# Optimization experiments

Measured on AMD Instinct MI355X. Metric: run time of the kernel, lower is better.

The kernel has to match this reference:

```python
import jax, jax.numpy as jnp
import numpy as np

N_ATOMS = 131072
N_ELEM = 4
D_IN = 128
D_HID = 256
D_OUT = 1


def setup_inputs() -> dict:
    key = jax.random.key(0)
    k1, k2, k3, k4, k5, k6 = jax.random.split(key, 6)
    descriptors = jax.random.normal(k1, (N_ATOMS, D_IN), dtype=jnp.float32)
    element_ids = jax.random.randint(k2, (N_ATOMS,), 0, N_ELEM, dtype=jnp.int32)
    # per-element 2-layer MLP params, stacked over the element (expert) axis
    s1 = 1.0 / np.sqrt(D_IN)
    s2 = 1.0 / np.sqrt(D_HID)
    W1 = jax.random.uniform(k3, (N_ELEM, D_IN, D_HID), minval=-s1, maxval=s1, dtype=jnp.float32)
    b1 = jax.random.uniform(k4, (N_ELEM, D_HID), minval=-s1, maxval=s1, dtype=jnp.float32)
    W2 = jax.random.uniform(k5, (N_ELEM, D_HID, D_OUT), minval=-s2, maxval=s2, dtype=jnp.float32)
    b2 = jax.random.uniform(k6, (N_ELEM, D_OUT), minval=-s2, maxval=s2, dtype=jnp.float32)
    return {"descriptors": descriptors, "element_ids": element_ids,
            "W1": W1, "b1": b1, "W2": W2, "b2": b2}


def reference(descriptors, element_ids, W1, b1, W2, b2):
    # Dense all-expert compute then per-atom select (E is tiny, avoids
    # materializing a per-atom gathered [N, D_IN, D_HID] weight tensor).
    h = jnp.tanh(jnp.einsum('ni,eih->neh', descriptors, W1) + b1[None])  # [N,E,H]
    y = jnp.einsum('neh,eho->neo', h, W2) + b2[None]                      # [N,E,O]
    idx = element_ids.astype(jnp.int32)[:, None, None]                    # [N,1,1]
    per_atom = jnp.take_along_axis(y, idx, axis=1)[:, 0, :]               # [N,O]
    total_energy = per_atom.sum(axis=0)                                   # [O]
    return total_energy
```

## Files before the change

### kernel.cpp

```cpp
#include <hip/hip_runtime.h>
#include <hip/hip_bf16.h>
#include <stdint.h>

#define N_ATOMS 131072
#define D_IN    128
#define D_HID   256
#define N_ELEM  4
#define NPAD    (N_ATOMS + N_ELEM * 64)
#define K4_BLOCKS 512
#define HIST_BLOCKS 128

typedef __attribute__((ext_vector_type(8))) short bf16x8;
typedef __attribute__((ext_vector_type(4))) float f32x4;
typedef unsigned long long ull;

#define WS_BPART  262272
#define WS_BCNT   278784
#define WS_SIDX   287232

__device__ __forceinline__ unsigned short f2bf_rne(float f) {
    union { float f; unsigned u; } v; v.f = f;
    unsigned r = v.u + 0x7FFFu + ((v.u >> 16) & 1u);
    return (unsigned short)(r >> 16);
}

__device__ __forceinline__ bf16x8 cvt8(f32x4 v0, f32x4 v1) {
    uint4 o;
    o.x = (__float_as_uint(v0[0]) >> 16) | (__float_as_uint(v0[1]) & 0xFFFF0000u);
    o.y = (__float_as_uint(v0[2]) >> 16) | (__float_as_uint(v0[3]) & 0xFFFF0000u);
    o.z = (__float_as_uint(v1[0]) >> 16) | (__float_as_uint(v1[1]) & 0xFFFF0000u);
    o.w = (__float_as_uint(v1[2]) >> 16) | (__float_as_uint(v1[3]) & 0xFFFF0000u);
    return __builtin_bit_cast(bf16x8, o);
}

__device__ __forceinline__ int4 wave_reduce4(int4 v) {
    #pragma unroll
    for (int off = 32; off; off >>= 1) {
        v.x += __shfl_xor(v.x, off);
        v.y += __shfl_xor(v.y, off);
        v.z += __shfl_xor(v.z, off);
        v.w += __shfl_xor(v.w, off);
    }
    return v;
}

__device__ __forceinline__ ull same_expert_mask(int e) {
    ull m0 = __ballot(e & 1);
    ull m1 = __ballot(e & 2);
    ull m = (e & 1) ? m0 : ~m0;
    return m & ((e & 2) ? m1 : ~m1);
}

__global__ void tnn_k1_fused(const int* __restrict__ eid, int* __restrict__ bcnt,
                             const float* __restrict__ W1, unsigned short* __restrict__ W1t) {
    __shared__ float tile[64][65];
    __shared__ int lc[N_ELEM];
    int t = threadIdx.x;
    if (blockIdx.x < 32) {
        int b  = blockIdx.x;
        int e  = b >> 3;
        int k0 = ((b >> 2) & 1) * 64;
        int h0 = (b & 3) * 64;
        int cg = t & 15;
        int rr = t >> 4;
        const float* src = W1 + ((size_t)e * D_IN + k0) * D_HID + h0;
        #pragma unroll
        for (int j = 0; j < 4; ++j) {
            int row = rr + j * 16;
            f32x4 v = *(const f32x4*)(src + (size_t)row * D_HID + cg * 4);
            tile[row][cg * 4 + 0] = v[0];
            tile[row][cg * 4 + 1] = v[1];
            tile[row][cg * 4 + 2] = v[2];
            tile[row][cg * 4 + 3] = v[3];
        }
        __syncthreads();
        unsigned short* dst = W1t + ((size_t)e * D_HID + h0) * D_IN + k0;
        #pragma unroll
        for (int j = 0; j < 4; ++j) {
            int hrow = rr + j * 16;
            ushort4 o;
            o.x = f2bf_rne(tile[cg * 4 + 0][hrow]);
            o.y = f2bf_rne(tile[cg * 4 + 1][hrow]);
            o.z = f2bf_rne(tile[cg * 4 + 2][hrow]);
            o.w = f2bf_rne(tile[cg * 4 + 3][hrow]);
            *(ushort4*)(dst + (size_t)hrow * D_IN + cg * 4) = o;
        }
    } else {
        int hb = blockIdx.x - 32;
        int lane = t & 63;
        if (t < N_ELEM) lc[t] = 0;
        __syncthreads();
        int base = hb * 1024;
        #pragma unroll
        for (int r = 0; r < 4; ++r) {
            int e = eid[base + r * 256 + t];
            ull m = same_expert_mask(e);
            if (lane == __builtin_ctzll(m))
                atomicAdd(&lc[e], __popcll(m));
        }
        __syncthreads();
        if (t < N_ELEM) bcnt[hb * 4 + t] = lc[t];
    }
}

__global__ void tnn_k3_scatter(const int* __restrict__ eid, const int* __restrict__ bcnt,
                               int* __restrict__ sortedIdx) {
    __shared__ int lc[N_ELEM];
    __shared__ int base4[N_ELEM];
    int t = threadIdx.x;
    int b = blockIdx.x;
    int lane = t & 63;
    if (t < N_ELEM) lc[t] = 0;
    if (t < 64) {
        int4 cl = ((const int4*)bcnt)[t];
        int4 ch = ((const int4*)bcnt)[t + 64];
        int4 tot = {cl.x + ch.x, cl.y + ch.y, cl.z + ch.z, cl.w + ch.w};
        tot = wave_reduce4(tot);
        int4 pre = {(t < b) ? cl.x : 0, (t < b) ? cl.y : 0,
                    (t < b) ? cl.z : 0, (t < b) ? cl.w : 0};
        if (t + 64 < b) { pre.x += ch.x; pre.y += ch.y; pre.z += ch.z; pre.w += ch.w; }
        pre = wave_reduce4(pre);
        if (t == 0) {
            int st0 = 0;
            int st1 = st0 + ((tot.x + 63) & ~63);
            int st2 = st1 + ((tot.y + 63) & ~63);
            int st3 = st2 + ((tot.z + 63) & ~63);
            base4[0] = st0 + pre.x;
            base4[1] = st1 + pre.y;
            base4[2] = st2 + pre.z;
            base4[3] = st3 + pre.w;
        }
    }
    __syncthreads();
    int base = b * 1024;
    ull below = (lane == 63) ? 0x7FFFFFFFFFFFFFFFULL : ((1ULL << lane) - 1);
    #pragma unroll
    for (int r = 0; r < 4; ++r) {
        int i = base + r * 256 + t;
        int e = eid[i];
        ull m = same_expert_mask(e);
        int f = __builtin_ctzll(m);
        int rank = __popcll(m & below);
        int wbase = 0;
        if (lane == f) wbase = atomicAdd(&lc[e], __popcll(m));
        wbase = __shfl(wbase, f);
        sortedIdx[base4[e] + wbase + rank] = i;
    }
}

template<bool FULL>
__device__ __forceinline__ float nt_loop(const unsigned char* ldsB, const float2* ldsBW,
                                         unsigned ldso, const bf16x8 a0[4], const bf16x8 a1[4],
                                         int tb, int rend, int lk, int l15, float fnval) {
    const float C2 = 2.8853900817779268f;
    float partial = 0.f;
    #pragma unroll 1
    for (int nt = 0; nt < 16; ++nt) {
        const unsigned char* lb = ldsB + ldso + (unsigned)nt * 256u;
        bf16x8 cur0 = *(const bf16x8*)(lb);
        bf16x8 cur1 = *(const bf16x8*)(lb + 16384);
        bf16x8 cur2 = *(const bf16x8*)(lb + 32768);
        bf16x8 cur3 = *(const bf16x8*)(lb + 49152);
        float2 bw = ldsBW[nt * 16 + l15];

        f32x4 acc0 = {0.f, 0.f, 0.f, 0.f};
        f32x4 acc1 = {0.f, 0.f, 0.f, 0.f};
        acc0 = __builtin_amdgcn_mfma_f32_16x16x32_bf16(a0[0], cur0, acc0, 0, 0, 0);
        acc1 = __builtin_amdgcn_mfma_f32_16x16x32_bf16(a1[0], cur0, acc1, 0, 0, 0);
        acc0 = __builtin_amdgcn_mfma_f32_16x16x32_bf16(a0[1], cur1, acc0, 0, 0, 0);
        acc1 = __builtin_amdgcn_mfma_f32_16x16x32_bf16(a1[1], cur1, acc1, 0, 0, 0);
        acc0 = __builtin_amdgcn_mfma_f32_16x16x32_bf16(a0[2], cur2, acc0, 0, 0, 0);
        acc1 = __builtin_amdgcn_mfma_f32_16x16x32_bf16(a1[2], cur2, acc1, 0, 0, 0);
        acc0 = __builtin_amdgcn_mfma_f32_16x16x32_bf16(a0[3], cur3, acc0, 0, 0, 0);
        acc1 = __builtin_amdgcn_mfma_f32_16x16x32_bf16(a1[3], cur3, acc1, 0, 0, 0);

        float rsum = 0.f;
        #pragma unroll
        for (int r = 0; r < 4; ++r) {
            float e0 = __builtin_amdgcn_exp2f(fmaf(C2, acc0[r], bw.x));
            float e1 = __builtin_amdgcn_exp2f(fmaf(C2, acc1[r], bw.x));
            float rc0 = __builtin_amdgcn_rcpf(e0 + 1.f);
            float rc1 = __builtin_amdgcn_rcpf(e1 + 1.f);
            if (!FULL) {
                rc0 = (tb + lk * 4 + r      < rend) ? rc0 : 0.f;
                rc1 = (tb + 16 + lk * 4 + r < rend) ? rc1 : 0.f;
            }
            rsum += rc0 + rc1;
        }
        partial = fmaf(bw.y, fmaf(-2.f, rsum, fnval), partial);
    }
    return partial;
}

__global__ __launch_bounds__(512, 4) void tnn_k4_mlp(
        const float* __restrict__ X, const int* __restrict__ sortedIdx,
        const int* __restrict__ bcnt, const unsigned short* __restrict__ W1t,
        const float* __restrict__ b1, const float* __restrict__ W2,
        float* __restrict__ bpart) {
    __shared__ unsigned char ldsB[65536];
    __shared__ float2 ldsBW[256];
    const float C2 = 2.8853900817779268f;

    int t = threadIdx.x;
    int wid  = t >> 6;
    int lane = t & 63;
    int l15  = lane & 15;
    int lk   = lane >> 4;
    int e    = blockIdx.x & 3;
    int q    = blockIdx.x >> 2;

    int4 cl = ((const int4*)bcnt)[lane];
    int4 ch = ((const int4*)bcnt)[lane + 64];
    int4 tot = {cl.x + ch.x, cl.y + ch.y, cl.z + ch.z, cl.w + ch.w};
    tot = wave_reduce4(tot);
    int cnts[4] = {tot.x, tot.y, tot.z, tot.w};
    int st[5];
    st[0] = 0;
    #pragma unroll
    for (int i = 0; i < 4; ++i) st[i + 1] = st[i] + ((cnts[i] + 63) & ~63);
    int bstart = st[e];
    int cnt    = cnts[e];
    int rend   = bstart + cnt;
    int Te     = (st[e + 1] - bstart) >> 5;
    int fb     = (cnt > 0) ? sortedIdx[bstart] : 0;

    {
        int hrow  = t >> 1;
        int khalf = t & 1;
        const unsigned short* src = W1t + ((size_t)e * D_HID + hrow) * D_IN + khalf * 64;
        #pragma unroll
        for (int jj = 0; jj < 8; ++jj) {
            bf16x8 v = *(const bf16x8*)(src + jj * 8);
            *(bf16x8*)(ldsB + (khalf * 8 + jj) * 4096 + hrow * 16) = v;
        }
        if (t < 256) ldsBW[t] = make_float2(b1[e * D_HID + t] * C2, W2[e * D_HID + t]);
    }
    __syncthreads();

    unsigned ldso = (unsigned)lk * 4096u + (unsigned)l15 * 16u;

    float partial = 0.f;
    for (int tt = q * 8 + wid; tt < Te; tt += 1024) {
        int tb = bstart + tt * 32;
        bool full = (tb + 32 <= rend);

        int slot0 = tb + l15, slot1 = slot0 + 16;
        int r0 = (slot0 < rend) ? sortedIdx[slot0] : fb;
        int r1 = (slot1 < rend) ? sortedIdx[slot1] : fb;

        bf16x8 a0[4], a1[4];
        const float* x0 = X + (size_t)r0 * D_IN + lk * 8;
        const float* x1 = X + (size_t)r1 * D_IN + lk * 8;
        #pragma unroll
        for (int ks = 0; ks < 4; ++ks)
            a0[ks] = cvt8(*(const f32x4*)(x0 + ks * 32), *(const f32x4*)(x0 + ks * 32 + 4));
        #pragma unroll
        for (int ks = 0; ks < 4; ++ks)
            a1[ks] = cvt8(*(const f32x4*)(x1 + ks * 32), *(const f32x4*)(x1 + ks * 32 + 4));

        if (full) {
            partial += nt_loop<true >(ldsB, ldsBW, ldso, a0, a1, tb, rend, lk, l15, 8.f);
        } else {
            int nv = 0;
            #pragma unroll
            for (int m = 0; m < 2; ++m)
                #pragma unroll
                for (int r = 0; r < 4; ++r)
                    nv += (tb + m * 16 + lk * 4 + r < rend) ? 1 : 0;
            partial += nt_loop<false>(ldsB, ldsBW, ldso, a0, a1, tb, rend, lk, l15, (float)nv);
        }
    }

    #pragma unroll
    for (int off = 32; off; off >>= 1)
        partial += __shfl_down(partial, off);
    if (lane == 0) bpart[blockIdx.x * 8 + wid] = partial;
}

__global__ void tnn_k5_reduce(const float* __restrict__ bpart, const int* __restrict__ bcnt,
                              const float* __restrict__ b2, float* __restrict__ out) {
    __shared__ float r[4];
    int t = threadIdx.x;
    float s = 0.f;
    #pragma unroll
    for (int j = 0; j < 16; ++j) s += bpart[j * 256 + t];
    #pragma unroll
    for (int off = 32; off; off >>= 1)
        s += __shfl_down(s, off);
    if ((t & 63) == 0) r[t >> 6] = s;
    __syncthreads();
    if (t < 64) {
        int4 cl = ((const int4*)bcnt)[t];
        int4 ch = ((const int4*)bcnt)[t + 64];
        int4 tot = {cl.x + ch.x, cl.y + ch.y, cl.z + ch.z, cl.w + ch.w};
        tot = wave_reduce4(tot);
        if (t == 0) {
            float acc = r[0] + r[1] + r[2] + r[3];
            acc += (float)tot.x * b2[0];
            acc += (float)tot.y * b2[1];
            acc += (float)tot.z * b2[2];
            acc += (float)tot.w * b2[3];
            out[0] = acc;
        }
    }
}

extern "C" void kernel_launch(void* const* d_in, const int* in_sizes, int n_in,
                              void* d_out, int out_size, void* d_ws, size_t ws_size,
                              hipStream_t stream) {
    const float* X   = (const float*)d_in[0];
    const int*   eid = (const int*)  d_in[1];
    const float* W1  = (const float*)d_in[2];
    const float* b1  = (const float*)d_in[3];
    const float* W2  = (const float*)d_in[4];
    const float* b2  = (const float*)d_in[5];
    float* out = (float*)d_out;

    char* ws = (char*)d_ws;
    unsigned short* W1t = (unsigned short*)ws;
    float* bpart     = (float*)(ws + WS_BPART);
    int*   bcnt      = (int*)  (ws + WS_BCNT);
    int*   sortedIdx = (int*)  (ws + WS_SIDX);

    hipLaunchKernelGGL(tnn_k1_fused,   dim3(32 + HIST_BLOCKS), dim3(256), 0, stream, eid, bcnt, W1, W1t);
    hipLaunchKernelGGL(tnn_k3_scatter, dim3(HIST_BLOCKS),      dim3(256), 0, stream, eid, bcnt, sortedIdx);
    hipLaunchKernelGGL(tnn_k4_mlp,     dim3(K4_BLOCKS),        dim3(512), 0, stream,
                       X, sortedIdx, bcnt, W1t, b1, W2, bpart);
    hipLaunchKernelGGL(tnn_k5_reduce,  dim3(1),                dim3(256), 0, stream, bpart, bcnt, b2, out);
}
```

Baseline: 37.88 us.

## Shrink MLP row tile to 16 and software-prefetch next tile's gathered rows

The per-wave row tile in the MoE MLP kernel shrinks from 32 to 16 atoms, so each tile now issues one MFMA chain instead of two. The loop is restructured to gather the next tile's raw fp32 descriptor rows into registers while the current tile's MFMA and tanh work runs, hiding gather latency. Workspace offsets move. The trade-off is half the weight reuse per LDS B-fragment load and twice as many tile iterations, plus extra registers for the prefetch buffer.

```diff
diff --git a/kernel.cpp b/kernel.cpp
--- a/kernel.cpp
+++ b/kernel.cpp
@@ -15,8 +15,8 @@
 typedef unsigned long long ull;
 
 #define WS_BPART  262272
-#define WS_BCNT   278784
-#define WS_SIDX   287232
+#define WS_BCNT   295168
+#define WS_SIDX   297472
 
 __device__ __forceinline__ unsigned short f2bf_rne(float f) {
     union { float f; unsigned u; } v; v.f = f;
@@ -149,9 +149,9 @@
 }
 
 template<bool FULL>
-__device__ __forceinline__ float nt_loop(const unsigned char* ldsB, const float2* ldsBW,
-                                         unsigned ldso, const bf16x8 a0[4], const bf16x8 a1[4],
-                                         int tb, int rend, int lk, int l15, float fnval) {
+__device__ __forceinline__ float nt_loop16(const unsigned char* ldsB, const float2* ldsBW,
+                                           unsigned ldso, const bf16x8 a[4],
+                                           int tb, int rend, int lk, int l15, float fnval) {
     const float C2 = 2.8853900817779268f;
     float partial = 0.f;
     #pragma unroll 1
@@ -163,31 +163,22 @@
         bf16x8 cur3 = *(const bf16x8*)(lb + 49152);
         float2 bw = ldsBW[nt * 16 + l15];
 
-        f32x4 acc0 = {0.f, 0.f, 0.f, 0.f};
-        f32x4 acc1 = {0.f, 0.f, 0.f, 0.f};
-        acc0 = __builtin_amdgcn_mfma_f32_16x16x32_bf16(a0[0], cur0, acc0, 0, 0, 0);
-        acc1 = __builtin_amdgcn_mfma_f32_16x16x32_bf16(a1[0], cur0, acc1, 0, 0, 0);
-        acc0 = __builtin_amdgcn_mfma_f32_16x16x32_bf16(a0[1], cur1, acc0, 0, 0, 0);
-        acc1 = __builtin_amdgcn_mfma_f32_16x16x32_bf16(a1[1], cur1, acc1, 0, 0, 0);
-        acc0 = __builtin_amdgcn_mfma_f32_16x16x32_bf16(a0[2], cur2, acc0, 0, 0, 0);
-        acc1 = __builtin_amdgcn_mfma_f32_16x16x32_bf16(a1[2], cur2, acc1, 0, 0, 0);
-        acc0 = __builtin_amdgcn_mfma_f32_16x16x32_bf16(a0[3], cur3, acc0, 0, 0, 0);
-        acc1 = __builtin_amdgcn_mfma_f32_16x16x32_bf16(a1[3], cur3, acc1, 0, 0, 0);
-
-        float rsum = 0.f;
+        f32x4 acc = {0.f, 0.f, 0.f, 0.f};
+        acc = __builtin_amdgcn_mfma_f32_16x16x32_bf16(a[0], cur0, acc, 0, 0, 0);
+        acc = __builtin_amdgcn_mfma_f32_16x16x32_bf16(a[1], cur1, acc, 0, 0, 0);
+        acc = __builtin_amdgcn_mfma_f32_16x16x32_bf16(a[2], cur2, acc, 0, 0, 0);
+        acc = __builtin_amdgcn_mfma_f32_16x16x32_bf16(a[3], cur3, acc, 0, 0, 0);
+
+        float rs0 = 0.f, rs1 = 0.f;
         #pragma unroll
         for (int r = 0; r < 4; ++r) {
-            float e0 = __builtin_amdgcn_exp2f(fmaf(C2, acc0[r], bw.x));
-            float e1 = __builtin_amdgcn_exp2f(fmaf(C2, acc1[r], bw.x));
-            float rc0 = __builtin_amdgcn_rcpf(e0 + 1.f);
-            float rc1 = __builtin_amdgcn_rcpf(e1 + 1.f);
-            if (!FULL) {
-                rc0 = (tb + lk * 4 + r      < rend) ? rc0 : 0.f;
-                rc1 = (tb + 16 + lk * 4 + r < rend) ? rc1 : 0.f;
-            }
-            rsum += rc0 + rc1;
-        }
-        partial = fmaf(bw.y, fmaf(-2.f, rsum, fnval), partial);
+            float ev = __builtin_amdgcn_exp2f(fmaf(C2, acc[r], bw.x));
+            float rc = __builtin_amdgcn_rcpf(ev + 1.f);
+            if (!FULL)
+                rc = (tb + lk * 4 + r < rend) ? rc : 0.f;
+            if (r & 1) rs1 += rc; else rs0 += rc;
+        }
+        partial = fmaf(bw.y, fmaf(-2.f, rs0 + rs1, fnval), partial);
     }
     return partial;
 }
@@ -211,8 +202,7 @@
 
     int4 cl = ((const int4*)bcnt)[lane];
     int4 ch = ((const int4*)bcnt)[lane + 64];
-    int4 tot = {cl.x + ch.x, cl.y + ch.y, cl.z + ch.z, cl.w + ch.w};
-    tot = wave_reduce4(tot);
+    int4 tot = wave_reduce4(int4{cl.x + ch.x, cl.y + ch.y, cl.z + ch.z, cl.w + ch.w});
     int cnts[4] = {tot.x, tot.y, tot.z, tot.w};
     int st[5];
     st[0] = 0;
@@ -221,7 +211,7 @@
     int bstart = st[e];
     int cnt    = cnts[e];
     int rend   = bstart + cnt;
-    int Te     = (st[e + 1] - bstart) >> 5;
+    int Te     = (st[e + 1] - bstart) >> 4;
     int fb     = (cnt > 0) ? sortedIdx[bstart] : 0;
 
     {
@@ -239,35 +229,48 @@
 
     unsigned ldso = (unsigned)lk * 4096u + (unsigned)l15 * 16u;
 
+    auto gather = [&](int tt, f32x4* raw) {
+        int tb = bstart + tt * 16;
+        int slot = tb + l15;
+        int row = (slot < rend) ? sortedIdx[slot] : fb;
+        const float* xr = X + (size_t)row * D_IN + lk * 8;
+        #pragma unroll
+        for (int ks = 0; ks < 4; ++ks) {
+            raw[2 * ks]     = *(const f32x4*)(xr + ks * 32);
+            raw[2 * ks + 1] = *(const f32x4*)(xr + ks * 32 + 4);
+        }
+    };
+
     float partial = 0.f;
-    for (int tt = q * 8 + wid; tt < Te; tt += 1024) {
-        int tb = bstart + tt * 32;
-        bool full = (tb + 32 <= rend);
-
-        int slot0 = tb + l15, slot1 = slot0 + 16;
-        int r0 = (slot0 < rend) ? sortedIdx[slot0] : fb;
-        int r1 = (slot1 < rend) ? sortedIdx[slot1] : fb;
-
-        bf16x8 a0[4], a1[4];
-        const float* x0 = X + (size_t)r0 * D_IN + lk * 8;
-        const float* x1 = X + (size_t)r1 * D_IN + lk * 8;
-        #pragma unroll
-        for (int ks = 0; ks < 4; ++ks)
-            a0[ks] = cvt8(*(const f32x4*)(x0 + ks * 32), *(const f32x4*)(x0 + ks * 32 + 4));
-        #pragma unroll
-        for (int ks = 0; ks < 4; ++ks)
-            a1[ks] = cvt8(*(const f32x4*)(x1 + ks * 32), *(const f32x4*)(x1 + ks * 32 + 4));
-
-        if (full) {
-            partial += nt_loop<true >(ldsB, ldsBW, ldso, a0, a1, tb, rend, lk, l15, 8.f);
-        } else {
-            int nv = 0;
+    {
+        int tt = q * 8 + wid;
+        f32x4 raw[8];
+        bool have = (tt < Te);
+        if (have) gather(tt, raw);
+        #pragma unroll 1
+        while (have) {
+            bf16x8 a[4];
             #pragma unroll
-            for (int m = 0; m < 2; ++m)
+            for (int ks = 0; ks < 4; ++ks)
+                a[ks] = cvt8(raw[2 * ks], raw[2 * ks + 1]);
+
+            int tb  = bstart + tt * 16;
+            int ttn = tt + 1024;
+            bool haveN = (ttn < Te);
+            if (haveN) gather(ttn, raw);
+
+            bool full = (tb + 16 <= rend);
+            if (full) {
+                partial += nt_loop16<true >(ldsB, ldsBW, ldso, a, tb, rend, lk, l15, 4.f);
+            } else {
+                int nv = 0;
                 #pragma unroll
                 for (int r = 0; r < 4; ++r)
-                    nv += (tb + m * 16 + lk * 4 + r < rend) ? 1 : 0;
-            partial += nt_loop<false>(ldsB, ldsBW, ldso, a0, a1, tb, rend, lk, l15, (float)nv);
+                    nv += (tb + lk * 4 + r < rend) ? 1 : 0;
+                partial += nt_loop16<false>(ldsB, ldsBW, ldso, a, tb, rend, lk, l15, (float)nv);
+            }
+            tt = ttn;
+            have = haveN;
         }
     }
 
@@ -322,9 +325,12 @@
     int*   bcnt      = (int*)  (ws + WS_BCNT);
     int*   sortedIdx = (int*)  (ws + WS_SIDX);
 
-    hipLaunchKernelGGL(tnn_k1_fused,   dim3(32 + HIST_BLOCKS), dim3(256), 0, stream, eid, bcnt, W1, W1t);
-    hipLaunchKernelGGL(tnn_k3_scatter, dim3(HIST_BLOCKS),      dim3(256), 0, stream, eid, bcnt, sortedIdx);
+    hipLaunchKernelGGL(tnn_k1_fused,   dim3(32 + HIST_BLOCKS), dim3(256), 0, stream,
+                       eid, bcnt, W1, W1t);
+    hipLaunchKernelGGL(tnn_k3_scatter, dim3(HIST_BLOCKS),      dim3(256), 0, stream,
+                       eid, bcnt, sortedIdx);
     hipLaunchKernelGGL(tnn_k4_mlp,     dim3(K4_BLOCKS),        dim3(512), 0, stream,
                        X, sortedIdx, bcnt, W1t, b1, W2, bpart);
-    hipLaunchKernelGGL(tnn_k5_reduce,  dim3(1),                dim3(256), 0, stream, bpart, bcnt, b2, out);
-}
+    hipLaunchKernelGGL(tnn_k5_reduce,  dim3(1),                dim3(256), 0, stream,
+                       bpart, bcnt, b2, out);
+}
```

Result: slower. 40.35 us (+6.5%).
